# Kernel tuning notes

Hardware: AMD Instinct MI355X
Metric: run time of the kernel (lower is better)

The kernel has to match this reference:

```python
import jax, jax.numpy as jnp
import numpy as np

B, S, E = 2, 2048, 1024
H = 16
HD = E // H  # 64


def setup_inputs() -> dict:
    key = jax.random.key(0)
    ks = jax.random.split(key, 9)
    sc = 1.0 / np.sqrt(E)
    return {
        "X": jax.random.normal(ks[0], (B, S, E), jnp.float32),
        "Wq": jax.random.normal(ks[1], (E, E), jnp.float32) * sc,
        "bq": jax.random.normal(ks[2], (E,), jnp.float32) * sc,
        "Wk": jax.random.normal(ks[3], (E, E), jnp.float32) * sc,
        "bk": jax.random.normal(ks[4], (E,), jnp.float32) * sc,
        "Wv": jax.random.normal(ks[5], (E, E), jnp.float32) * sc,
        "bv": jax.random.normal(ks[6], (E,), jnp.float32) * sc,
        "Wo": jax.random.normal(ks[7], (E, E), jnp.float32) * sc,
        "bo": jax.random.normal(ks[8], (E,), jnp.float32) * sc,
    }


def reference(X, Wq, bq, Wk, bk, Wv, bv, Wo, bo):
    b, s, e = X.shape
    # torch Linear: x @ W.T + b (weights stored (out, in))
    Q = X @ Wq.T + bq
    K = X @ Wk.T + bk
    V = X @ Wv.T + bv
    # (b, s, E) -> (b, H, s, HD)
    Q = Q.reshape(b, s, H, HD).transpose(0, 2, 1, 3)
    K = K.reshape(b, s, H, HD).transpose(0, 2, 1, 3)
    V = V.reshape(b, s, H, HD).transpose(0, 2, 1, 3)
    scores = jnp.einsum("bhqd,bhkd->bhqk", Q, K) / np.sqrt(HD).astype(np.float32)
    attn = jax.nn.softmax(scores, axis=-1)
    ctx = jnp.einsum("bhqk,bhkd->bhqd", attn, V)  # (b, H, s, HD)
    # Faithful to original: reshape (b,H,s,HD) -> (b,s,E) WITHOUT permuting heads back
    ctx = ctx.reshape(b, s, e)
    return ctx @ Wo.T + bo
```

## Files before the change

### kernel.cpp

```cpp
#include <hip/hip_runtime.h>


typedef __bf16 bf16x8 __attribute__((ext_vector_type(8)));
typedef __bf16 bf16x4 __attribute__((ext_vector_type(4)));
typedef float f32x4 __attribute__((ext_vector_type(4)));
typedef unsigned short ushort_t;

#define S_LEN 2048
#define E_DIM 1024
#define H_NUM 16
#define HD_DIM 64

#if __has_builtin(__builtin_amdgcn_exp2f)
#define EXP2(x) __builtin_amdgcn_exp2f(x)
#else
#define EXP2(x) __exp2f(x)
#endif

__device__ __forceinline__ ushort_t f2bf(float f) {
  union { float f; unsigned u; } v; v.f = f;
  unsigned u = v.u;
  unsigned r = (u + 0x7FFFu + ((u >> 16) & 1u)) >> 16;
  return (ushort_t)r;
}

#define GLDS16(gp, lp)                                              \
  __builtin_amdgcn_global_load_lds(                                 \
      (const __attribute__((address_space(1))) unsigned int*)(gp),  \
      (__attribute__((address_space(3))) unsigned int*)(lp), 16, 0, 0)

__global__ __launch_bounds__(256) void cvt_all(
    const float* __restrict__ X, const float* __restrict__ Wq,
    const float* __restrict__ Wk, const float* __restrict__ Wv,
    const float* __restrict__ Wo, ushort_t* __restrict__ Xbf,
    ushort_t* __restrict__ Wqkv, ushort_t* __restrict__ Wob) {
  int i = blockIdx.x * 256 + threadIdx.x;
  const float* src;
  ushort_t* dst;
  int off;
  if (i < 1048576) {
    src = X; dst = Xbf; off = i;
  } else if (i < 1310720) {
    src = Wq; dst = Wqkv; off = i - 1048576;
  } else if (i < 1572864) {
    src = Wk; dst = Wqkv + (1 << 20); off = i - 1310720;
  } else if (i < 1835008) {
    src = Wv; dst = Wqkv + (2 << 20); off = i - 1572864;
  } else {
    src = Wo; dst = Wob; off = i - 1835008;
  }
  float4 v = ((const float4*)src)[off];
  ushort4 o;
  o.x = f2bf(v.x); o.y = f2bf(v.y); o.z = f2bf(v.z); o.w = f2bf(v.w);
  ((ushort4*)dst)[off] = o;
}

__global__ __launch_bounds__(256) void gemm_qkv(
    const ushort_t* __restrict__ Xbf, const ushort_t* __restrict__ Wqkv,
    const float* __restrict__ bq, const float* __restrict__ bk,
    const float* __restrict__ bv,
    ushort_t* __restrict__ Qb, ushort_t* __restrict__ Kb,
    ushort_t* __restrict__ Vt) {
  __shared__ ushort_t smem[16384];
  ushort_t* As = smem;
  ushort_t* Bs = smem + 8192;
  const int t = threadIdx.x;
  const int w = t >> 6, lane = t & 63, quad = lane >> 4, lr = lane & 15;
  const int m0 = blockIdx.y * 128, n0 = blockIdx.x * 128;
  const int wm = (w & 1) * 64, wn = (w >> 1) * 64;
  const int matid = n0 >> 10;
  const int nl0 = n0 & 1023;

  const int srow = t >> 3;
  const int gsrc = (t & 7) ^ (srow & 7);
  const ushort_t* Ag = Xbf + (size_t)(m0 + srow) * E_DIM + gsrc * 8;
  const ushort_t* Bg = Wqkv + (size_t)matid * E_DIM * E_DIM +
                       (size_t)(nl0 + srow) * E_DIM + gsrc * 8;

  f32x4 acc[4][4] = {};

  for (int kt = 0; kt < E_DIM / 64; ++kt) {
#pragma unroll
    for (int r = 0; r < 4; r++) {
      GLDS16(Ag + (size_t)r * 32 * E_DIM, As + r * 2048 + t * 8);
      GLDS16(Bg + (size_t)r * 32 * E_DIM, Bs + r * 2048 + t * 8);
    }
    Ag += 64; Bg += 64;
    __syncthreads();
#pragma unroll
    for (int kk = 0; kk < 2; kk++) {
      bf16x8 af[4], bfr[4];
      const int gs0 = (kk * 4 + quad) ^ (lr & 7);
#pragma unroll
      for (int i = 0; i < 4; i++) {
        af[i]  = *(const bf16x8*)(As + (wm + i * 16 + lr) * 64 + gs0 * 8);
        bfr[i] = *(const bf16x8*)(Bs + (wn + i * 16 + lr) * 64 + gs0 * 8);
      }
      if (matid < 2) {
#pragma unroll
        for (int i = 0; i < 4; i++)
#pragma unroll
          for (int j = 0; j < 4; j++)
            acc[i][j] = __builtin_amdgcn_mfma_f32_16x16x32_bf16(
                bfr[j], af[i], acc[i][j], 0, 0, 0);
      } else {
#pragma unroll
        for (int i = 0; i < 4; i++)
#pragma unroll
          for (int j = 0; j < 4; j++)
            acc[i][j] = __builtin_amdgcn_mfma_f32_16x16x32_bf16(
                af[i], bfr[j], acc[i][j], 0, 0, 0);
      }
    }
    __syncthreads();
  }

  const float* bias_p = (matid == 0) ? bq : (matid == 1) ? bk : bv;
  ushort_t* Ls = smem;
  if (matid < 2) {
    ushort_t* dst = (matid == 0) ? Qb : Kb;
    const float scl = (matid == 0) ? 0.18033688f : 1.0f;
#pragma unroll
    for (int j = 0; j < 4; j++) {
      const int nb = wn + j * 16 + quad * 4;
      float b0 = bias_p[nl0 + nb], b1 = bias_p[nl0 + nb + 1];
      float b2 = bias_p[nl0 + nb + 2], b3 = bias_p[nl0 + nb + 3];
#pragma unroll
      for (int i = 0; i < 4; i++) {
        const int m = wm + i * 16 + lr;
        bf16x4 pv;
        pv[0] = (__bf16)((acc[i][j][0] + b0) * scl);
        pv[1] = (__bf16)((acc[i][j][1] + b1) * scl);
        pv[2] = (__bf16)((acc[i][j][2] + b2) * scl);
        pv[3] = (__bf16)((acc[i][j][3] + b3) * scl);
        *(bf16x4*)(Ls + m * 128 + (((nb >> 3) ^ (m & 7)) * 8) + (nb & 7)) = pv;
      }
    }
    __syncthreads();
#pragma unroll
    for (int it = 0; it < 8; it++) {
      const int task = t + 256 * it;
      const int m = task >> 4, g = task & 15;
      uint4 val = *(const uint4*)(Ls + m * 128 + ((g ^ (m & 7)) * 8));
      const int s = m0 + m, bb = s >> 11, ss = s & 2047;
      const int cl = nl0 + g * 8, h = cl >> 6, dd = cl & 63;
      *(uint4*)(dst + ((size_t)((bb * H_NUM + h) * S_LEN + ss)) * HD_DIM + dd) =
          val;
    }
  } else {
#pragma unroll
    for (int j = 0; j < 4; j++) {
      const int n = wn + j * 16 + lr;
      const float bias = bias_p[nl0 + n];
#pragma unroll
      for (int i = 0; i < 4; i++) {
        const int mb = wm + i * 16 + quad * 4;
        bf16x4 pv;
        pv[0] = (__bf16)(acc[i][j][0] + bias);
        pv[1] = (__bf16)(acc[i][j][1] + bias);
        pv[2] = (__bf16)(acc[i][j][2] + bias);
        pv[3] = (__bf16)(acc[i][j][3] + bias);
        *(bf16x4*)(Ls + n * 128 + (((mb >> 3) ^ (n & 7)) * 8) + (mb & 7)) = pv;
      }
    }
    __syncthreads();
    const int n = t & 127, grp = t >> 7;
    ushort_t v[64];
#pragma unroll
    for (int c = 0; c < 8; c++)
      *(uint4*)(v + c * 8) =
          *(const uint4*)(Ls + n * 128 + (((grp * 8 + c) ^ (n & 7)) * 8));
    const int cl = nl0 + n, h = cl >> 6, dd = cl & 63;
    const int sgb = m0 + grp * 64, bb = sgb >> 11, ssb = sgb & 2047;
    ushort_t* dstp =
        Vt + ((size_t)((bb * H_NUM + h) * HD_DIM + dd)) * S_LEN + ssb;
#pragma unroll
    for (int q = 0; q < 8; q++) {
      ushort_t o8[8];
#pragma unroll
      for (int u = 0; u < 8; u++) o8[u] = v[16 * (u & 3) + 2 * q + (u >> 2)];
      *(uint4*)(dstp + q * 8) = *(const uint4*)o8;
    }
  }
}

__global__ __launch_bounds__(256) void attn(
    const ushort_t* __restrict__ Qb, const ushort_t* __restrict__ Kb,
    const ushort_t* __restrict__ Vt, ushort_t* __restrict__ Ctx) {
  __shared__ ushort_t Ks[64 * 64];
  __shared__ ushort_t Vs[64 * 64];
  __shared__ ushort_t Ps[128 * 72];
  const int t = threadIdx.x, w = t >> 6, lane = t & 63;
  const int quad = lane >> 4, lr = lane & 15;
  const int bh = blockIdx.y, q0 = blockIdx.x * 128;
  const ushort_t* Qg = Qb + ((size_t)bh * S_LEN + q0) * HD_DIM;
  const ushort_t* Kg = Kb + (size_t)bh * S_LEN * HD_DIM;
  const ushort_t* Vg = Vt + (size_t)bh * HD_DIM * S_LEN;

  const int srow = t >> 3;
  const int gsrc = (t & 7) ^ (srow & 7);

#pragma unroll
  for (int r = 0; r < 4; r++)
    GLDS16(Qg + (size_t)(r * 32 + srow) * HD_DIM + gsrc * 8,
           Ps + r * 2048 + t * 8);
#pragma unroll
  for (int r = 0; r < 2; r++) {
    GLDS16(Kg + (size_t)(r * 32 + srow) * HD_DIM + gsrc * 8,
           Ks + r * 2048 + t * 8);
    GLDS16(Vg + (size_t)(r * 32 + srow) * S_LEN + gsrc * 8,
           Vs + r * 2048 + t * 8);
  }
  __syncthreads();
  bf16x8 qf[2][2];
#pragma unroll
  for (int mt = 0; mt < 2; mt++)
#pragma unroll
    for (int kc = 0; kc < 2; kc++) {
      int gs = (kc * 4 + quad) ^ (lr & 7);
      qf[mt][kc] =
          *(const bf16x8*)(Ps + (w * 32 + mt * 16 + lr) * 64 + gs * 8);
    }

  bf16x8 ones;
#pragma unroll
  for (int e = 0; e < 8; e++) ones[e] = (__bf16)1.0f;

  f32x4 cacc[2][4] = {};
  f32x4 lsum[2] = {};

  for (int kt = 0; kt < S_LEN / 64; ++kt) {
    f32x4 sacc[2][4] = {};
#pragma unroll
    for (int nt = 0; nt < 4; nt++) {
#pragma unroll
      for (int kc = 0; kc < 2; kc++) {
        int gs = (kc * 4 + quad) ^ (lr & 7);
        bf16x8 kf = *(const bf16x8*)(Ks + (nt * 16 + lr) * 64 + gs * 8);
        sacc[0][nt] = __builtin_amdgcn_mfma_f32_16x16x32_bf16(
            qf[0][kc], kf, sacc[0][nt], 0, 0, 0);
        sacc[1][nt] = __builtin_amdgcn_mfma_f32_16x16x32_bf16(
            qf[1][kc], kf, sacc[1][nt], 0, 0, 0);
      }
    }
    __syncthreads();

    const int kn = (kt + 1) & (S_LEN / 64 - 1);
#pragma unroll
    for (int r = 0; r < 2; r++)
      GLDS16(Kg + (size_t)(kn * 64 + r * 32 + srow) * HD_DIM + gsrc * 8,
             Ks + r * 2048 + t * 8);

#pragma unroll
    for (int mt = 0; mt < 2; mt++) {
#pragma unroll
      for (int i = 0; i < 4; i++) {
        float p0 = EXP2(sacc[mt][0][i]);
        float p1 = EXP2(sacc[mt][1][i]);
        float p2 = EXP2(sacc[mt][2][i]);
        float p3 = EXP2(sacc[mt][3][i]);
        bf16x4 pv;
        pv[0] = (__bf16)p0; pv[1] = (__bf16)p1;
        pv[2] = (__bf16)p2; pv[3] = (__bf16)p3;
        int row = w * 32 + mt * 16 + quad * 4 + i;
        *(bf16x4*)(Ps + row * 72 + lr * 4) = pv;
      }
    }

#pragma unroll
    for (int kc = 0; kc < 2; kc++) {
      int gs = (kc * 4 + quad) ^ (lr & 7);
      bf16x8 vf[4];
#pragma unroll
      for (int dt = 0; dt < 4; dt++)
        vf[dt] = *(const bf16x8*)(Vs + (dt * 16 + lr) * 64 + gs * 8);
#pragma unroll
      for (int mt = 0; mt < 2; mt++) {
        bf16x8 pf = *(const bf16x8*)(Ps + (w * 32 + mt * 16 + lr) * 72 +
                                     kc * 32 + quad * 8);
        lsum[mt] =
            __builtin_amdgcn_mfma_f32_16x16x32_bf16(pf, ones, lsum[mt], 0, 0, 0);
#pragma unroll
        for (int dt = 0; dt < 4; dt++)
          cacc[mt][dt] = __builtin_amdgcn_mfma_f32_16x16x32_bf16(
              pf, vf[dt], cacc[mt][dt], 0, 0, 0);
      }
    }
    __syncthreads();

#pragma unroll
    for (int r = 0; r < 2; r++)
      GLDS16(Vg + (size_t)(r * 32 + srow) * S_LEN + kn * 64 + gsrc * 8,
             Vs + r * 2048 + t * 8);
  }

#pragma unroll
  for (int mt = 0; mt < 2; mt++) {
#pragma unroll
    for (int i = 0; i < 4; i++) {
      float inv = 1.0f / lsum[mt][i];
      int srow2 = q0 + w * 32 + mt * 16 + quad * 4 + i;
#pragma unroll
      for (int dt = 0; dt < 4; dt++)
        Ctx[((size_t)bh * S_LEN + srow2) * HD_DIM + dt * 16 + lr] =
            f2bf(cacc[mt][dt][i] * inv);
    }
  }
}

__global__ __launch_bounds__(256) void gemm_out(
    const ushort_t* __restrict__ Cb, const ushort_t* __restrict__ Wob,
    const float* __restrict__ bo, float* __restrict__ out) {
  __shared__ ushort_t As[128 * 64];
  __shared__ ushort_t Bs[64 * 64];
  const int t = threadIdx.x;
  const int w = t >> 6, lane = t & 63, quad = lane >> 4, lr = lane & 15;
  const int m0 = blockIdx.y * 128, n0 = blockIdx.x * 64;
  const int wm = (w & 1) * 64, wn = (w >> 1) * 32;

  const int srow = t >> 3;
  const int gsrc = (t & 7) ^ (srow & 7);
  const ushort_t* Ag = Cb + (size_t)(m0 + srow) * E_DIM + gsrc * 8;
  const ushort_t* Bg = Wob + (size_t)(n0 + srow) * E_DIM + gsrc * 8;

  f32x4 acc[4][2] = {};

  for (int kt = 0; kt < E_DIM / 64; ++kt) {
#pragma unroll
    for (int r = 0; r < 4; r++)
      GLDS16(Ag + (size_t)r * 32 * E_DIM, As + r * 2048 + t * 8);
#pragma unroll
    for (int r = 0; r < 2; r++)
      GLDS16(Bg + (size_t)r * 32 * E_DIM, Bs + r * 2048 + t * 8);
    Ag += 64; Bg += 64;
    __syncthreads();
#pragma unroll
    for (int kk = 0; kk < 2; kk++) {
      bf16x8 af[4], bfr[2];
      const int gs0 = (kk * 4 + quad) ^ (lr & 7);
#pragma unroll
      for (int i = 0; i < 4; i++)
        af[i] = *(const bf16x8*)(As + (wm + i * 16 + lr) * 64 + gs0 * 8);
#pragma unroll
      for (int j = 0; j < 2; j++)
        bfr[j] = *(const bf16x8*)(Bs + (wn + j * 16 + lr) * 64 + gs0 * 8);
#pragma unroll
      for (int i = 0; i < 4; i++)
#pragma unroll
        for (int j = 0; j < 2; j++)
          acc[i][j] = __builtin_amdgcn_mfma_f32_16x16x32_bf16(
              af[i], bfr[j], acc[i][j], 0, 0, 0);
    }
    __syncthreads();
  }

#pragma unroll
  for (int j = 0; j < 2; j++) {
    int col = n0 + wn + j * 16 + lr;
    float bias = bo[col];
#pragma unroll
    for (int i = 0; i < 4; i++) {
#pragma unroll
      for (int r = 0; r < 4; r++) {
        int row = m0 + wm + i * 16 + quad * 4 + r;
        out[(size_t)row * E_DIM + col] = acc[i][j][r] + bias;
      }
    }
  }
}

extern "C" void kernel_launch(void* const* d_in, const int* in_sizes, int n_in,
                              void* d_out, int out_size, void* d_ws,
                              size_t ws_size, hipStream_t stream) {
  const float* X  = (const float*)d_in[0];
  const float* bq = (const float*)d_in[2];
  const float* bk = (const float*)d_in[4];
  const float* bv = (const float*)d_in[6];
  const float* Wo = (const float*)d_in[7];
  const float* bo = (const float*)d_in[8];
  float* out = (float*)d_out;

  char* ws = (char*)d_ws;
  ushort_t* Xbf  = (ushort_t*)(ws);
  ushort_t* Wqkv = (ushort_t*)(ws + ((size_t)8 << 20));
  ushort_t* Wob  = (ushort_t*)(ws + ((size_t)14 << 20));
  ushort_t* Qb   = (ushort_t*)(ws + ((size_t)16 << 20));
  ushort_t* Kb   = (ushort_t*)(ws + ((size_t)24 << 20));
  ushort_t* Vt   = (ushort_t*)(ws + ((size_t)32 << 20));
  ushort_t* Cb   = (ushort_t*)(ws + ((size_t)40 << 20));

  cvt_all<<<8192, 256, 0, stream>>>(X, (const float*)d_in[1],
                                    (const float*)d_in[3],
                                    (const float*)d_in[5], Wo, Xbf, Wqkv, Wob);

  gemm_qkv<<<dim3(24, 32), 256, 0, stream>>>(Xbf, Wqkv, bq, bk, bv, Qb, Kb, Vt);
  attn<<<dim3(16, 32), 256, 0, stream>>>(Qb, Kb, Vt, Cb);
  gemm_out<<<dim3(16, 32), 256, 0, stream>>>(Cb, Wob, bo, out);
}
```

Before: 195.4 us.

## Split attention over key halves with combine pass, swizzle GEMM block order

The attention kernel now splits the key/value range into two halves across a third grid dimension, writing unnormalized fp32 partial context and row sums that a new combine kernel adds, normalizes and converts to bf16. This doubles the attention grid from 512 to 1024 blocks to fill more compute units, at the cost of an extra kernel launch and fp32 partial traffic. Both GEMMs also switch to a 1D grid with grouped block ordering (8 row tiles per group) to improve L2 reuse of the weight tiles. Workspace buffers are reshuffled so that the partials alias regions already consumed.

```diff
diff --git a/kernel.cpp b/kernel.cpp
--- a/kernel.cpp
+++ b/kernel.cpp
@@ -66,7 +66,9 @@
   ushort_t* Bs = smem + 8192;
   const int t = threadIdx.x;
   const int w = t >> 6, lane = t & 63, quad = lane >> 4, lr = lane & 15;
-  const int m0 = blockIdx.y * 128, n0 = blockIdx.x * 128;
+  const int bid = blockIdx.x;
+  const int grp = bid / 192, rr = bid % 192;
+  const int m0 = (grp * 8 + (rr & 7)) * 128, n0 = (rr >> 3) * 128;
   const int wm = (w & 1) * 64, wn = (w >> 1) * 64;
   const int matid = n0 >> 10;
   const int nl0 = n0 & 1023;
@@ -164,14 +166,14 @@
       }
     }
     __syncthreads();
-    const int n = t & 127, grp = t >> 7;
+    const int n = t & 127, grp2 = t >> 7;
     ushort_t v[64];
 #pragma unroll
     for (int c = 0; c < 8; c++)
       *(uint4*)(v + c * 8) =
-          *(const uint4*)(Ls + n * 128 + (((grp * 8 + c) ^ (n & 7)) * 8));
+          *(const uint4*)(Ls + n * 128 + (((grp2 * 8 + c) ^ (n & 7)) * 8));
     const int cl = nl0 + n, h = cl >> 6, dd = cl & 63;
-    const int sgb = m0 + grp * 64, bb = sgb >> 11, ssb = sgb & 2047;
+    const int sgb = m0 + grp2 * 64, bb = sgb >> 11, ssb = sgb & 2047;
     ushort_t* dstp =
         Vt + ((size_t)((bb * H_NUM + h) * HD_DIM + dd)) * S_LEN + ssb;
 #pragma unroll
@@ -186,19 +188,21 @@
 
 __global__ __launch_bounds__(256) void attn(
     const ushort_t* __restrict__ Qb, const ushort_t* __restrict__ Kb,
-    const ushort_t* __restrict__ Vt, ushort_t* __restrict__ Ctx) {
+    const ushort_t* __restrict__ Vt, float* __restrict__ Pctx,
+    float* __restrict__ Plsum) {
   __shared__ ushort_t Ks[64 * 64];
   __shared__ ushort_t Vs[64 * 64];
   __shared__ ushort_t Ps[128 * 72];
   const int t = threadIdx.x, w = t >> 6, lane = t & 63;
   const int quad = lane >> 4, lr = lane & 15;
-  const int bh = blockIdx.y, q0 = blockIdx.x * 128;
+  const int bh = blockIdx.y, q0 = blockIdx.x * 128, z = blockIdx.z;
   const ushort_t* Qg = Qb + ((size_t)bh * S_LEN + q0) * HD_DIM;
   const ushort_t* Kg = Kb + (size_t)bh * S_LEN * HD_DIM;
   const ushort_t* Vg = Vt + (size_t)bh * HD_DIM * S_LEN;
 
   const int srow = t >> 3;
   const int gsrc = (t & 7) ^ (srow & 7);
+  const int kbase = z * 1024;
 
 #pragma unroll
   for (int r = 0; r < 4; r++)
@@ -206,9 +210,9 @@
            Ps + r * 2048 + t * 8);
 #pragma unroll
   for (int r = 0; r < 2; r++) {
-    GLDS16(Kg + (size_t)(r * 32 + srow) * HD_DIM + gsrc * 8,
+    GLDS16(Kg + (size_t)(kbase + r * 32 + srow) * HD_DIM + gsrc * 8,
            Ks + r * 2048 + t * 8);
-    GLDS16(Vg + (size_t)(r * 32 + srow) * S_LEN + gsrc * 8,
+    GLDS16(Vg + (size_t)(r * 32 + srow) * S_LEN + kbase + gsrc * 8,
            Vs + r * 2048 + t * 8);
   }
   __syncthreads();
@@ -229,7 +233,7 @@
   f32x4 cacc[2][4] = {};
   f32x4 lsum[2] = {};
 
-  for (int kt = 0; kt < S_LEN / 64; ++kt) {
+  for (int kt = 0; kt < 16; ++kt) {
     f32x4 sacc[2][4] = {};
 #pragma unroll
     for (int nt = 0; nt < 4; nt++) {
@@ -245,10 +249,10 @@
     }
     __syncthreads();
 
-    const int kn = (kt + 1) & (S_LEN / 64 - 1);
+    const int kn = kbase + (((kt + 1) & 15) << 6);
 #pragma unroll
     for (int r = 0; r < 2; r++)
-      GLDS16(Kg + (size_t)(kn * 64 + r * 32 + srow) * HD_DIM + gsrc * 8,
+      GLDS16(Kg + (size_t)(kn + r * 32 + srow) * HD_DIM + gsrc * 8,
              Ks + r * 2048 + t * 8);
 
 #pragma unroll
@@ -290,22 +294,39 @@
 
 #pragma unroll
     for (int r = 0; r < 2; r++)
-      GLDS16(Vg + (size_t)(r * 32 + srow) * S_LEN + kn * 64 + gsrc * 8,
+      GLDS16(Vg + (size_t)(r * 32 + srow) * S_LEN + kn + gsrc * 8,
              Vs + r * 2048 + t * 8);
   }
 
+  float* Pz = Pctx + (size_t)z * 4194304 + (size_t)bh * S_LEN * HD_DIM;
+  float* Lz = Plsum + z * 65536 + bh * S_LEN;
 #pragma unroll
   for (int mt = 0; mt < 2; mt++) {
 #pragma unroll
     for (int i = 0; i < 4; i++) {
-      float inv = 1.0f / lsum[mt][i];
       int srow2 = q0 + w * 32 + mt * 16 + quad * 4 + i;
+      if (lr == 0) Lz[srow2] = lsum[mt][i];
 #pragma unroll
       for (int dt = 0; dt < 4; dt++)
-        Ctx[((size_t)bh * S_LEN + srow2) * HD_DIM + dt * 16 + lr] =
-            f2bf(cacc[mt][dt][i] * inv);
-    }
-  }
+        Pz[(size_t)srow2 * HD_DIM + dt * 16 + lr] = cacc[mt][dt][i];
+    }
+  }
+}
+
+__global__ __launch_bounds__(256) void combine(
+    const float* __restrict__ Pctx, const float* __restrict__ Plsum,
+    ushort_t* __restrict__ Cb) {
+  int gid = blockIdx.x * 256 + threadIdx.x;
+  int row = gid >> 4;
+  float4 c0 = ((const float4*)Pctx)[gid];
+  float4 c1 = ((const float4*)(Pctx + (size_t)4194304))[gid];
+  float inv = 1.0f / (Plsum[row] + Plsum[65536 + row]);
+  bf16x4 o;
+  o[0] = (__bf16)((c0.x + c1.x) * inv);
+  o[1] = (__bf16)((c0.y + c1.y) * inv);
+  o[2] = (__bf16)((c0.z + c1.z) * inv);
+  o[3] = (__bf16)((c0.w + c1.w) * inv);
+  *(bf16x4*)(Cb + (size_t)gid * 4) = o;
 }
 
 __global__ __launch_bounds__(256) void gemm_out(
@@ -315,7 +336,9 @@
   __shared__ ushort_t Bs[64 * 64];
   const int t = threadIdx.x;
   const int w = t >> 6, lane = t & 63, quad = lane >> 4, lr = lane & 15;
-  const int m0 = blockIdx.y * 128, n0 = blockIdx.x * 64;
+  const int bid = blockIdx.x;
+  const int grp = bid >> 7, rr = bid & 127;
+  const int m0 = (grp * 8 + (rr & 7)) * 128, n0 = (rr >> 3) * 64;
   const int wm = (w & 1) * 64, wn = (w >> 1) * 32;
 
   const int srow = t >> 3;
@@ -381,19 +404,22 @@
   float* out = (float*)d_out;
 
   char* ws = (char*)d_ws;
-  ushort_t* Xbf  = (ushort_t*)(ws);
-  ushort_t* Wqkv = (ushort_t*)(ws + ((size_t)8 << 20));
-  ushort_t* Wob  = (ushort_t*)(ws + ((size_t)14 << 20));
-  ushort_t* Qb   = (ushort_t*)(ws + ((size_t)16 << 20));
-  ushort_t* Kb   = (ushort_t*)(ws + ((size_t)24 << 20));
-  ushort_t* Vt   = (ushort_t*)(ws + ((size_t)32 << 20));
-  ushort_t* Cb   = (ushort_t*)(ws + ((size_t)40 << 20));
+  ushort_t* Qb    = (ushort_t*)(ws);
+  ushort_t* Cb    = (ushort_t*)(ws);
+  ushort_t* Kb    = (ushort_t*)(ws + ((size_t)8 << 20));
+  ushort_t* Vt    = (ushort_t*)(ws + ((size_t)16 << 20));
+  ushort_t* Wob   = (ushort_t*)(ws + ((size_t)24 << 20));
+  ushort_t* Xbf   = (ushort_t*)(ws + ((size_t)26 << 20));
+  ushort_t* Wqkv  = (ushort_t*)(ws + ((size_t)34 << 20));
+  float*    Pctx  = (float*)(ws + ((size_t)26 << 20));
+  float*    Plsum = (float*)(ws + ((size_t)58 << 20));
 
   cvt_all<<<8192, 256, 0, stream>>>(X, (const float*)d_in[1],
                                     (const float*)d_in[3],
                                     (const float*)d_in[5], Wo, Xbf, Wqkv, Wob);
 
-  gemm_qkv<<<dim3(24, 32), 256, 0, stream>>>(Xbf, Wqkv, bq, bk, bv, Qb, Kb, Vt);
-  attn<<<dim3(16, 32), 256, 0, stream>>>(Qb, Kb, Vt, Cb);
-  gemm_out<<<dim3(16, 32), 256, 0, stream>>>(Cb, Wob, bo, out);
-}
+  gemm_qkv<<<768, 256, 0, stream>>>(Xbf, Wqkv, bq, bk, bv, Qb, Kb, Vt);
+  attn<<<dim3(16, 32, 2), 256, 0, stream>>>(Qb, Kb, Vt, Pctx, Plsum);
+  combine<<<4096, 256, 0, stream>>>(Pctx, Plsum, Cb);
+  gemm_out<<<512, 256, 0, stream>>>(Cb, Wob, bo, out);
+}
```

After: 204.4 us. 1.05x slower.

## Prefetch next K tile during MFMA and swizzle block order in GEMMs

Applied to the files above, without the earlier changes.

In both projection GEMMs, each K tile's LDS fragments are now read into registers first, then the next tile's global-to-LDS loads are issued before the MFMAs run, so memory latency overlaps compute within one shared buffer. The launch grids become 1D and are remapped so groups of 8 M-tiles share the same N-tile, for better L2 reuse of weights. Launch bounds request 3 blocks per CU. The trade-off is more register pressure from holding both k-halves of fragments and an extra barrier per iteration.

```diff
diff --git a/kernel.cpp b/kernel.cpp
--- a/kernel.cpp
+++ b/kernel.cpp
@@ -55,7 +55,7 @@
   ((ushort4*)dst)[off] = o;
 }
 
-__global__ __launch_bounds__(256) void gemm_qkv(
+__global__ __launch_bounds__(256, 3) void gemm_qkv(
     const ushort_t* __restrict__ Xbf, const ushort_t* __restrict__ Wqkv,
     const float* __restrict__ bq, const float* __restrict__ bk,
     const float* __restrict__ bv,
@@ -66,7 +66,9 @@
   ushort_t* Bs = smem + 8192;
   const int t = threadIdx.x;
   const int w = t >> 6, lane = t & 63, quad = lane >> 4, lr = lane & 15;
-  const int m0 = blockIdx.y * 128, n0 = blockIdx.x * 128;
+  const int bid = blockIdx.x;
+  const int grp = bid / 192, rr = bid % 192;
+  const int m0 = (grp * 8 + (rr & 7)) * 128, n0 = (rr >> 3) * 128;
   const int wm = (w & 1) * 64, wn = (w >> 1) * 64;
   const int matid = n0 >> 10;
   const int nl0 = n0 & 1023;
@@ -77,42 +79,55 @@
   const ushort_t* Bg = Wqkv + (size_t)matid * E_DIM * E_DIM +
                        (size_t)(nl0 + srow) * E_DIM + gsrc * 8;
 
+#pragma unroll
+  for (int r = 0; r < 4; r++) {
+    GLDS16(Ag + (size_t)r * 32 * E_DIM, As + r * 2048 + t * 8);
+    GLDS16(Bg + (size_t)r * 32 * E_DIM, Bs + r * 2048 + t * 8);
+  }
+  Ag += 64; Bg += 64;
+
   f32x4 acc[4][4] = {};
 
   for (int kt = 0; kt < E_DIM / 64; ++kt) {
-#pragma unroll
-    for (int r = 0; r < 4; r++) {
-      GLDS16(Ag + (size_t)r * 32 * E_DIM, As + r * 2048 + t * 8);
-      GLDS16(Bg + (size_t)r * 32 * E_DIM, Bs + r * 2048 + t * 8);
-    }
-    Ag += 64; Bg += 64;
-    __syncthreads();
+    __syncthreads();
+    bf16x8 af[2][4], bfr[2][4];
 #pragma unroll
     for (int kk = 0; kk < 2; kk++) {
-      bf16x8 af[4], bfr[4];
       const int gs0 = (kk * 4 + quad) ^ (lr & 7);
 #pragma unroll
       for (int i = 0; i < 4; i++) {
-        af[i]  = *(const bf16x8*)(As + (wm + i * 16 + lr) * 64 + gs0 * 8);
-        bfr[i] = *(const bf16x8*)(Bs + (wn + i * 16 + lr) * 64 + gs0 * 8);
-      }
-      if (matid < 2) {
+        af[kk][i]  = *(const bf16x8*)(As + (wm + i * 16 + lr) * 64 + gs0 * 8);
+        bfr[kk][i] = *(const bf16x8*)(Bs + (wn + i * 16 + lr) * 64 + gs0 * 8);
+      }
+    }
+    __syncthreads();
+    if (kt + 1 < E_DIM / 64) {
+#pragma unroll
+      for (int r = 0; r < 4; r++) {
+        GLDS16(Ag + (size_t)r * 32 * E_DIM, As + r * 2048 + t * 8);
+        GLDS16(Bg + (size_t)r * 32 * E_DIM, Bs + r * 2048 + t * 8);
+      }
+      Ag += 64; Bg += 64;
+    }
+    if (matid < 2) {
+#pragma unroll
+      for (int kk = 0; kk < 2; kk++)
 #pragma unroll
         for (int i = 0; i < 4; i++)
 #pragma unroll
           for (int j = 0; j < 4; j++)
             acc[i][j] = __builtin_amdgcn_mfma_f32_16x16x32_bf16(
-                bfr[j], af[i], acc[i][j], 0, 0, 0);
-      } else {
+                bfr[kk][j], af[kk][i], acc[i][j], 0, 0, 0);
+    } else {
+#pragma unroll
+      for (int kk = 0; kk < 2; kk++)
 #pragma unroll
         for (int i = 0; i < 4; i++)
 #pragma unroll
           for (int j = 0; j < 4; j++)
             acc[i][j] = __builtin_amdgcn_mfma_f32_16x16x32_bf16(
-                af[i], bfr[j], acc[i][j], 0, 0, 0);
-      }
-    }
-    __syncthreads();
+                af[kk][i], bfr[kk][j], acc[i][j], 0, 0, 0);
+    }
   }
 
   const float* bias_p = (matid == 0) ? bq : (matid == 1) ? bk : bv;
@@ -164,14 +179,14 @@
       }
     }
     __syncthreads();
-    const int n = t & 127, grp = t >> 7;
+    const int n = t & 127, grp2 = t >> 7;
     ushort_t v[64];
 #pragma unroll
     for (int c = 0; c < 8; c++)
       *(uint4*)(v + c * 8) =
-          *(const uint4*)(Ls + n * 128 + (((grp * 8 + c) ^ (n & 7)) * 8));
+          *(const uint4*)(Ls + n * 128 + (((grp2 * 8 + c) ^ (n & 7)) * 8));
     const int cl = nl0 + n, h = cl >> 6, dd = cl & 63;
-    const int sgb = m0 + grp * 64, bb = sgb >> 11, ssb = sgb & 2047;
+    const int sgb = m0 + grp2 * 64, bb = sgb >> 11, ssb = sgb & 2047;
     ushort_t* dstp =
         Vt + ((size_t)((bb * H_NUM + h) * HD_DIM + dd)) * S_LEN + ssb;
 #pragma unroll
@@ -308,14 +323,16 @@
   }
 }
 
-__global__ __launch_bounds__(256) void gemm_out(
+__global__ __launch_bounds__(256, 3) void gemm_out(
     const ushort_t* __restrict__ Cb, const ushort_t* __restrict__ Wob,
     const float* __restrict__ bo, float* __restrict__ out) {
   __shared__ ushort_t As[128 * 64];
   __shared__ ushort_t Bs[64 * 64];
   const int t = threadIdx.x;
   const int w = t >> 6, lane = t & 63, quad = lane >> 4, lr = lane & 15;
-  const int m0 = blockIdx.y * 128, n0 = blockIdx.x * 64;
+  const int bid = blockIdx.x;
+  const int grp = bid >> 7, rr = bid & 127;
+  const int m0 = (grp * 8 + (rr & 7)) * 128, n0 = (rr >> 3) * 64;
   const int wm = (w & 1) * 64, wn = (w >> 1) * 32;
 
   const int srow = t >> 3;
@@ -323,35 +340,47 @@
   const ushort_t* Ag = Cb + (size_t)(m0 + srow) * E_DIM + gsrc * 8;
   const ushort_t* Bg = Wob + (size_t)(n0 + srow) * E_DIM + gsrc * 8;
 
+#pragma unroll
+  for (int r = 0; r < 4; r++)
+    GLDS16(Ag + (size_t)r * 32 * E_DIM, As + r * 2048 + t * 8);
+#pragma unroll
+  for (int r = 0; r < 2; r++)
+    GLDS16(Bg + (size_t)r * 32 * E_DIM, Bs + r * 2048 + t * 8);
+  Ag += 64; Bg += 64;
+
   f32x4 acc[4][2] = {};
 
   for (int kt = 0; kt < E_DIM / 64; ++kt) {
-#pragma unroll
-    for (int r = 0; r < 4; r++)
-      GLDS16(Ag + (size_t)r * 32 * E_DIM, As + r * 2048 + t * 8);
-#pragma unroll
-    for (int r = 0; r < 2; r++)
-      GLDS16(Bg + (size_t)r * 32 * E_DIM, Bs + r * 2048 + t * 8);
-    Ag += 64; Bg += 64;
-    __syncthreads();
+    __syncthreads();
+    bf16x8 af[2][4], bfr[2][2];
 #pragma unroll
     for (int kk = 0; kk < 2; kk++) {
-      bf16x8 af[4], bfr[2];
       const int gs0 = (kk * 4 + quad) ^ (lr & 7);
 #pragma unroll
       for (int i = 0; i < 4; i++)
-        af[i] = *(const bf16x8*)(As + (wm + i * 16 + lr) * 64 + gs0 * 8);
+        af[kk][i] = *(const bf16x8*)(As + (wm + i * 16 + lr) * 64 + gs0 * 8);
 #pragma unroll
       for (int j = 0; j < 2; j++)
-        bfr[j] = *(const bf16x8*)(Bs + (wn + j * 16 + lr) * 64 + gs0 * 8);
+        bfr[kk][j] = *(const bf16x8*)(Bs + (wn + j * 16 + lr) * 64 + gs0 * 8);
+    }
+    __syncthreads();
+    if (kt + 1 < E_DIM / 64) {
+#pragma unroll
+      for (int r = 0; r < 4; r++)
+        GLDS16(Ag + (size_t)r * 32 * E_DIM, As + r * 2048 + t * 8);
+#pragma unroll
+      for (int r = 0; r < 2; r++)
+        GLDS16(Bg + (size_t)r * 32 * E_DIM, Bs + r * 2048 + t * 8);
+      Ag += 64; Bg += 64;
+    }
+#pragma unroll
+    for (int kk = 0; kk < 2; kk++)
 #pragma unroll
       for (int i = 0; i < 4; i++)
 #pragma unroll
         for (int j = 0; j < 2; j++)
           acc[i][j] = __builtin_amdgcn_mfma_f32_16x16x32_bf16(
-              af[i], bfr[j], acc[i][j], 0, 0, 0);
-    }
-    __syncthreads();
+              af[kk][i], bfr[kk][j], acc[i][j], 0, 0, 0);
   }
 
 #pragma unroll
@@ -393,7 +422,7 @@
                                     (const float*)d_in[3],
                                     (const float*)d_in[5], Wo, Xbf, Wqkv, Wob);
 
-  gemm_qkv<<<dim3(24, 32), 256, 0, stream>>>(Xbf, Wqkv, bq, bk, bv, Qb, Kb, Vt);
+  gemm_qkv<<<768, 256, 0, stream>>>(Xbf, Wqkv, bq, bk, bv, Qb, Kb, Vt);
   attn<<<dim3(16, 32), 256, 0, stream>>>(Qb, Kb, Vt, Cb);
-  gemm_out<<<dim3(16, 32), 256, 0, stream>>>(Cb, Wob, bo, out);
-}
+  gemm_out<<<512, 256, 0, stream>>>(Cb, Wob, bo, out);
+}
```

New measurement: 294.7 us. 1.51x slower.
